# Optimization experiments

Measured on AMD Instinct MI355X. Metric: run time of the kernel, lower is better.

The kernel has to match this reference:

```python
import jax, jax.numpy as jnp
import numpy as np
import math

B, N, D = 8, 4096, 768
H, M, L = 12, 64, 4
HD = D // H  # 64
TEMP = 1.0
EPS = 1e-5


def layer_norm(x, g, b):
    m = jnp.mean(x, axis=-1, keepdims=True)
    v = jnp.mean((x - m) ** 2, axis=-1, keepdims=True)
    return (x - m) * jax.lax.rsqrt(v + EPS) * g + b


def setup_inputs() -> dict:
    key = jax.random.key(0)
    ks = jax.random.split(key, 24)
    s = 0.02
    inp = {
        "latent_tokens": jax.random.normal(ks[0], (B, N, D), jnp.float32),
        "selector": jax.random.normal(ks[1], (M, D), jnp.float32) * s,
        "qc": jax.random.normal(ks[2], (L, M, D), jnp.float32) * s,
        "qw": jax.random.normal(ks[3], (L, H, D, HD), jnp.float32) * s,
        "qb": jnp.zeros((L, H, HD), jnp.float32),
        "kw": jax.random.normal(ks[4], (L, H, D, HD), jnp.float32) * s,
        "kb": jnp.zeros((L, H, HD), jnp.float32),
        "vw": jax.random.normal(ks[5], (L, H, D, HD), jnp.float32) * s,
        "vb": jnp.zeros((L, H, HD), jnp.float32),
        "hw": jax.random.normal(ks[6], (L, H, HD, HD), jnp.float32) * s,
        "hb": jnp.zeros((L, H, HD), jnp.float32),
        "ow": jax.random.normal(ks[7], (L, D, D), jnp.float32) * s,
        "ob": jnp.zeros((L, D), jnp.float32),
        "w1": jax.random.normal(ks[8], (L, D, 4 * D), jnp.float32) * s,
        "b1": jnp.zeros((L, 4 * D), jnp.float32),
        "w2": jax.random.normal(ks[9], (L, 4 * D, D), jnp.float32) * s,
        "b2": jnp.zeros((L, D), jnp.float32),
        "g1": jnp.ones((L, D), jnp.float32),
        "beta1": jnp.zeros((L, D), jnp.float32),
        "g2": jnp.ones((L, D), jnp.float32),
        "beta2": jnp.zeros((L, D), jnp.float32),
    }
    return inp


def reference(latent_tokens, selector, qc, qw, qb, kw, kb, vw, vb, hw, hb,
              ow, ob, w1, b1, w2, b2, g1, beta1, g2, beta2):
    scale = 1.0 / math.sqrt(HD)
    # soft-selection pooling of encoder tokens into M pos queries
    logits = jnp.einsum('bnd,md->bmn', latent_tokens, selector)
    weights = jax.nn.softmax(logits / TEMP, axis=-1)
    x = jnp.einsum('bmn,bnd->bmd', weights, latent_tokens)  # [B,M,D]
    for l in range(L):
        queries = qc[l][None] + x                                    # [B,M,D]
        q = jnp.einsum('bmd,hde->bhme', queries, qw[l]) + qb[l][None, :, None, :]
        k = jnp.einsum('bnd,hde->bhne', latent_tokens, kw[l]) + kb[l][None, :, None, :]
        v = jnp.einsum('bnd,hde->bhne', latent_tokens, vw[l]) + vb[l][None, :, None, :]
        attn = jax.nn.softmax(jnp.einsum('bhme,bhne->bhmn', q, k) * scale, axis=-1)
        o = jnp.einsum('bhmn,bhne->bhme', attn, v)                   # [B,H,M,HD]
        o = jnp.einsum('bhme,hef->bhmf', o, hw[l]) + hb[l][None, :, None, :]
        o = o.transpose(0, 2, 1, 3).reshape(o.shape[0], M, D)        # concat heads
        o = o @ ow[l] + ob[l]
        x1 = layer_norm(o + queries, g1[l], beta1[l])
        mlp = jax.nn.gelu(x1 @ w1[l] + b1[l], approximate=False) @ w2[l] + b2[l]
        x = layer_norm(x1 + mlp, g2[l], beta2[l])
    return x
```

## Files before the change

kernel.cpp:

```cpp
#include <hip/hip_runtime.h>
#include <hip/hip_bf16.h>


using bf16 = __hip_bfloat16;
typedef __attribute__((ext_vector_type(8))) __bf16 bf16x8;
typedef __attribute__((ext_vector_type(4))) float f32x4;
typedef unsigned int u32;
typedef __attribute__((ext_vector_type(4))) u32 u32x4;

#define DEVINL __device__ __forceinline__

DEVINL float bf2f(bf16 v) { return __bfloat162float(v); }
DEVINL bf16 f2bf(float v) { return __float2bfloat16(v); }
DEVINL u32 f2bfu(float f) { bf16 h = __float2bfloat16(f); return *(unsigned short*)&h; }
DEVINL float gelu_f(float x) { return 0.5f * x * (1.0f + erff(x * 0.70710678118654752f)); }

DEVINL void async16(const bf16* g, bf16* l) {
  __builtin_amdgcn_global_load_lds(
      (const __attribute__((address_space(1))) u32*)g,
      (__attribute__((address_space(3))) u32*)l, 16, 0, 0);
}

DEVINL u32 xcd_swizzle(u32 id, u32 nwg) {
  u32 q = nwg >> 3, r = nwg & 7;
  u32 xcd = id & 7, pos = id >> 3;
  return xcd * q + (xcd < r ? xcd : r) + pos;
}

__global__ __launch_bounds__(256) void cvt_f2b(const float* in, bf16* out, long n) {
  const long i = ((long)blockIdx.x * 256 + threadIdx.x) * 8;
  if (i >= n) return;
  float4 a = *(const float4*)(in + i);
  float4 b = *(const float4*)(in + i + 4);
  u32 w[4];
  w[0] = f2bfu(a.x) | (f2bfu(a.y) << 16);
  w[1] = f2bfu(a.z) | (f2bfu(a.w) << 16);
  w[2] = f2bfu(b.x) | (f2bfu(b.y) << 16);
  w[3] = f2bfu(b.z) | (f2bfu(b.w) << 16);
  *(u32x4*)(out + i) = *(u32x4*)w;
}

struct GemmKVP {
  const bf16* A;
  const bf16* Bk;
  const bf16* Bv;
  bf16* Ck;
  bf16* Cv;
  const float* biask;
  const float* biasv;
};

__global__ __launch_bounds__(512, 4) void gemm_kv(GemmKVP p) {
  __shared__ __align__(16) bf16 SH[36864];
  bf16* As = SH;
  bf16* Ks = SH + 12288;
  bf16* Vs = SH + 24576;
  const int tid = threadIdx.x;
  const int wave = tid >> 6, lane = tid & 63;

  u32 id = blockIdx.x + 6u * blockIdx.y;
  id = xcd_swizzle(id, 1536);
  const int bn = id % 6;
  const int bm = id / 6;

  const bf16* Ag = p.A + (long)bm * 128 * 768;
  const bf16* Kg = p.Bk + (long)bn * 128 * 768;
  const bf16* Vg = p.Bv + (long)bn * 128 * 768;

  const int cq = (((tid & 3) ^ ((tid >> 3) & 3))) * 8;
  const long ro = (long)(tid >> 2) * 768 + cq;
  const bf16* ga = Ag + ro;
  const bf16* gk = Kg + ro;
  const bf16* gv = Vg + ro;

  const int m_in = lane & 15, q = lane >> 4;
  const int wstream = wave >> 2;
  const int wq = wave & 3;
  const int wm = (wq & 1) * 64, wn = (wq >> 1) * 64;
  const int sw3 = (q ^ ((m_in >> 1) & 3)) << 3;
  f32x4 acc[4][4] = {};
  const int nk = 24;

  auto stage = [&](int s, int ko) {
    async16(ga + ko, As + s * 4096 + tid * 8);
    async16(gk + ko, Ks + s * 4096 + tid * 8);
    async16(gv + ko, Vs + s * 4096 + tid * 8);
  };
  stage(0, 0);
  stage(1, 32);

  for (int k = 0; k < nk; ++k) {
    if (k + 1 < nk) asm volatile("s_waitcnt vmcnt(3)" ::: "memory");
    else            asm volatile("s_waitcnt vmcnt(0)" ::: "memory");
    __builtin_amdgcn_s_barrier();
    if (k + 2 < nk) stage((k + 2) % 3, (k + 2) * 32);
    const bf16* Ac = As + (k % 3) * 4096;
    const bf16* Bc = (wstream == 0 ? Ks : Vs) + (k % 3) * 4096;
    bf16x8 af[4], bfr[4];
#pragma unroll
    for (int i = 0; i < 4; i++)
      af[i] = *(const bf16x8*)(Ac + (wm + i * 16 + m_in) * 32 + sw3);
#pragma unroll
    for (int j = 0; j < 4; j++)
      bfr[j] = *(const bf16x8*)(Bc + (wn + j * 16 + m_in) * 32 + sw3);
#pragma unroll
    for (int i = 0; i < 4; i++)
#pragma unroll
      for (int j = 0; j < 4; j++)
        acc[i][j] = __builtin_amdgcn_mfma_f32_16x16x32_bf16(af[i], bfr[j], acc[i][j], 0, 0, 0);
  }

  const int bb = (bm * 128) >> 12;
  const int nn0 = (bm * 128) & 4095;
  __syncthreads();
  if (wstream == 0) {
    const long row0 = (long)bm * 128 + wm + q * 4;
    const long col0 = (long)bn * 128 + wn + m_in;
#pragma unroll
    for (int i = 0; i < 4; i++)
#pragma unroll
      for (int j = 0; j < 4; j++) {
        long r = row0 + i * 16;
        long c = col0 + j * 16;
        float bk_ = p.biask[c];
#pragma unroll
        for (int t = 0; t < 4; t++)
          p.Ck[(r + t) * 768 + c] = f2bf(acc[i][j][t] + bk_);
      }
  } else {
    bf16* VT = SH;
#pragma unroll
    for (int i = 0; i < 4; i++) {
      const int nb = wm + q * 4 + i * 16;
      const int sl = nb >> 3;
      const int of = nb & 7;
#pragma unroll
      for (int j = 0; j < 4; j++) {
        const int e = wn + j * 16 + m_in;
        const float bv_ = p.biasv[bn * 128 + e];
        u32 w0 = f2bfu(acc[i][j][0] + bv_) | (f2bfu(acc[i][j][1] + bv_) << 16);
        u32 w1 = f2bfu(acc[i][j][2] + bv_) | (f2bfu(acc[i][j][3] + bv_) << 16);
        uint2 pk; pk.x = w0; pk.y = w1;
        *(uint2*)(VT + e * 128 + ((sl ^ (e & 15)) << 3) + of) = pk;
      }
    }
  }
  __syncthreads();
  bf16* CvB = p.Cv + (long)bb * 3145728;
  const bf16* VT = SH;
#pragma unroll
  for (int k2 = 0; k2 < 4; k2++) {
    int g = tid + k2 * 512;
    int e = g >> 4, sc = g & 15;
    u32x4 vv = *(const u32x4*)(VT + e * 128 + ((sc ^ (e & 15)) << 3));
    *(u32x4*)(CvB + (long)(bn * 128 + e) * 4096 + nn0 + sc * 8) = vv;
  }
}

struct GemmSmP {
  const bf16* A; const bf16* B; void* C; const float* bias; const float* res;
  long sA1, sA2, sB1, sB2, sC1, sC2, sBias2;
  int nb2, lda, ldb, ldc, K;
  int bias_mode;
  int out_mode;
  float scale;
};

__global__ __launch_bounds__(256, 4) void gemm_sm(GemmSmP p) {
  __shared__ __align__(16) bf16 As[3][64 * 32];
  __shared__ __align__(16) bf16 Bs[3][64 * 32];
  const int tid = threadIdx.x;
  const int wave = tid >> 6, lane = tid & 63;

  const u32 gx = gridDim.x, gy = gridDim.y;
  u32 id = blockIdx.x + gx * (blockIdx.y + gy * blockIdx.z);
  id = xcd_swizzle(id, gx * gy * gridDim.z);
  const int bn = id % gx;
  const u32 t2 = id / gx;
  const int bm = t2 % gy;
  const int bz = t2 / gy;

  const int z1 = bz / p.nb2, z2 = bz - z1 * p.nb2;
  const bf16* Ag = p.A + p.sA1 * z1 + p.sA2 * z2 + (long)bm * 64 * p.lda;
  const bf16* Bg = p.B + p.sB1 * z1 + p.sB2 * z2 + (long)bn * 64 * p.ldb;

  const int cq = (((tid & 3) ^ ((tid >> 3) & 3))) * 8;
  const bf16* gpa = Ag + ((long)(tid >> 2) * p.lda + cq);
  const bf16* gpb = Bg + ((long)(tid >> 2) * p.ldb + cq);

  const int m_in = lane & 15, q = lane >> 4;
  const int wm = (wave & 1) * 32, wn = (wave >> 1) * 32;
  const int sw3 = (q ^ ((m_in >> 1) & 3)) << 3;
  f32x4 acc[2][2] = {};
  const int nk = p.K >> 5;

  async16(gpa, &As[0][0] + tid * 8);
  async16(gpb, &Bs[0][0] + tid * 8);
  if (nk > 1) {
    async16(gpa + 32, &As[1][0] + tid * 8);
    async16(gpb + 32, &Bs[1][0] + tid * 8);
  }

  int slot = 0;
  for (int k = 0; k < nk; ++k) {
    if (k + 1 < nk) asm volatile("s_waitcnt vmcnt(2)" ::: "memory");
    else            asm volatile("s_waitcnt vmcnt(0)" ::: "memory");
    __builtin_amdgcn_s_barrier();
    if (k + 2 < nk) {
      int ns = slot + 2; if (ns >= 3) ns -= 3;
      const int ko = (k + 2) * 32;
      async16(gpa + ko, &As[ns][0] + tid * 8);
      async16(gpb + ko, &Bs[ns][0] + tid * 8);
    }
    const bf16* Ac = &As[slot][0];
    const bf16* Bc = &Bs[slot][0];
    bf16x8 a0 = *(const bf16x8*)(Ac + (wm + m_in) * 32 + sw3);
    bf16x8 a1 = *(const bf16x8*)(Ac + (wm + 16 + m_in) * 32 + sw3);
    bf16x8 b0 = *(const bf16x8*)(Bc + (wn + m_in) * 32 + sw3);
    bf16x8 b1 = *(const bf16x8*)(Bc + (wn + 16 + m_in) * 32 + sw3);
    acc[0][0] = __builtin_amdgcn_mfma_f32_16x16x32_bf16(a0, b0, acc[0][0], 0, 0, 0);
    acc[0][1] = __builtin_amdgcn_mfma_f32_16x16x32_bf16(a0, b1, acc[0][1], 0, 0, 0);
    acc[1][0] = __builtin_amdgcn_mfma_f32_16x16x32_bf16(a1, b0, acc[1][0], 0, 0, 0);
    acc[1][1] = __builtin_amdgcn_mfma_f32_16x16x32_bf16(a1, b1, acc[1][1], 0, 0, 0);
    slot = (slot + 1 == 3) ? 0 : slot + 1;
  }

  const long row0 = (long)bm * 64 + wm + q * 4;
  const long col0 = (long)bn * 64 + wn + m_in;
  const float* bias = p.bias + p.sBias2 * z2;
#pragma unroll
  for (int i = 0; i < 2; i++)
#pragma unroll
    for (int j = 0; j < 2; j++) {
      long r = row0 + i * 16;
      long cc = col0 + j * 16;
      float badd = (p.bias_mode == 1) ? bias[cc] : 0.f;
#pragma unroll
      for (int t = 0; t < 4; t++) {
        float v = acc[i][j][t] * p.scale + badd;
        long idx = (r + t) * p.ldc + cc;
        if (p.out_mode == 0) {
          float* Cf = (float*)p.C + p.sC1 * z1 + p.sC2 * z2;
          if (p.res) v += p.res[idx];
          Cf[idx] = v;
        } else {
          bf16* Cb = (bf16*)p.C + p.sC1 * z1 + p.sC2 * z2;
          if (p.out_mode == 2) v = gelu_f(v);
          Cb[idx] = f2bf(v);
        }
      }
    }
}

struct AttnP {
  const bf16* Q;
  const bf16* K;
  const bf16* VT;
  float* Opart;
  float* ML;
};

__global__ __launch_bounds__(256, 3) void attn_part(AttnP p) {
  __shared__ __align__(16) bf16 SH[24576];
  bf16* Qs = SH;
  bf16* Ks = SH + 4096;
  bf16* Vs = SH + 12288;
  bf16* Ps = SH + 20480;
  const int tid = threadIdx.x;
  const int wave = tid >> 6, lane = tid & 63;
  const int z = blockIdx.x, c = blockIdx.y;
  const int b = z / 12, h = z - b * 12;
  const int n0 = c * 512;

  const int sl0 = tid, sl1 = tid + 256;
  const int r0 = sl0 >> 3, r1 = sl1 >> 3;
  const int q0 = (sl0 & 7) ^ (r0 & 7), q1 = (sl1 & 7) ^ (r1 & 7);

  const bf16* Qg = p.Q + ((long)b * 64) * 768 + h * 64;
  const bf16* Kg = p.K + ((long)b * 4096 + n0) * 768 + h * 64;
  const bf16* Vg = p.VT + (long)b * 3145728 + (long)(h * 64) * 4096 + n0;

  async16(Qg + (long)r0 * 768 + q0 * 8, Qs + sl0 * 8);
  async16(Qg + (long)r1 * 768 + q1 * 8, Qs + sl1 * 8);
  auto stageK = [&](int s) {
    bf16* d = Ks + (s & 1) * 4096;
    async16(Kg + (long)(s * 64 + r0) * 768 + q0 * 8, d + sl0 * 8);
    async16(Kg + (long)(s * 64 + r1) * 768 + q1 * 8, d + sl1 * 8);
  };
  auto stageV = [&](int s) {
    bf16* d = Vs + (s & 1) * 4096;
    async16(Vg + (long)r0 * 4096 + s * 64 + q0 * 8, d + sl0 * 8);
    async16(Vg + (long)r1 * 4096 + s * 64 + q1 * 8, d + sl1 * 8);
  };
  stageK(0); stageV(0); stageK(1); stageV(1);

  const int m_in = lane & 15, q = lane >> 4;
  const int wm = wave * 16;

  asm volatile("s_waitcnt vmcnt(8)" ::: "memory");
  __builtin_amdgcn_s_barrier();

  bf16x8 qa[2];
  {
    const int ra = wm + m_in;
#pragma unroll
    for (int kk = 0; kk < 2; kk++)
      qa[kk] = *(const bf16x8*)(Qs + ra * 64 + ((((kk * 4 + q) ^ (ra & 7))) << 3));
  }

  f32x4 accO[4] = {};
  float m_run[4] = {-1e30f, -1e30f, -1e30f, -1e30f};
  float l_run[4] = {0.f, 0.f, 0.f, 0.f};

  for (int s = 0; s < 8; ++s) {
    if (s < 7) asm volatile("s_waitcnt vmcnt(4)" ::: "memory");
    else       asm volatile("s_waitcnt vmcnt(0)" ::: "memory");
    __builtin_amdgcn_s_barrier();
    const bf16* Kc = Ks + (s & 1) * 4096;
    const bf16* Vc = Vs + (s & 1) * 4096;
    f32x4 accS[4] = {};
#pragma unroll
    for (int kk = 0; kk < 2; kk++) {
#pragma unroll
      for (int j = 0; j < 4; j++) {
        const int rj = j * 16 + m_in;
        bf16x8 kb = *(const bf16x8*)(Kc + rj * 64 + ((((kk * 4 + q) ^ (rj & 7))) << 3));
        accS[j] = __builtin_amdgcn_mfma_f32_16x16x32_bf16(qa[kk], kb, accS[j], 0, 0, 0);
      }
    }
    float pe[4][4], osc[4];
#pragma unroll
    for (int t = 0; t < 4; t++) {
      float mx = fmaxf(fmaxf(accS[0][t], accS[1][t]), fmaxf(accS[2][t], accS[3][t])) * 0.125f;
      mx = fmaxf(mx, __shfl_xor(mx, 1));
      mx = fmaxf(mx, __shfl_xor(mx, 2));
      mx = fmaxf(mx, __shfl_xor(mx, 4));
      mx = fmaxf(mx, __shfl_xor(mx, 8));
      const float mnew = fmaxf(m_run[t], mx);
      const float so = __expf(m_run[t] - mnew);
      float rs = 0.f;
#pragma unroll
      for (int j = 0; j < 4; j++) {
        float e = __expf(accS[j][t] * 0.125f - mnew);
        pe[j][t] = e; rs += e;
      }
      rs += __shfl_xor(rs, 1); rs += __shfl_xor(rs, 2);
      rs += __shfl_xor(rs, 4); rs += __shfl_xor(rs, 8);
      l_run[t] = l_run[t] * so + rs;
      m_run[t] = mnew;
      osc[t] = so;
    }
#pragma unroll
    for (int ef = 0; ef < 4; ef++)
#pragma unroll
      for (int t = 0; t < 4; t++) accO[ef][t] *= osc[t];
#pragma unroll
    for (int j = 0; j < 4; j++) {
      const int pc = m_in + 16 * j;
#pragma unroll
      for (int t = 0; t < 4; t++) {
        const int pm = wm + q * 4 + t;
        Ps[pm * 64 + (((pc >> 3) ^ (pm & 7)) << 3) + (pc & 7)] = f2bf(pe[j][t]);
      }
    }
    const int ra = wm + m_in;
#pragma unroll
    for (int kk = 0; kk < 2; kk++) {
      bf16x8 pa = *(const bf16x8*)(Ps + ra * 64 + ((((kk * 4 + q) ^ (ra & 7))) << 3));
#pragma unroll
      for (int ef = 0; ef < 4; ef++) {
        const int rv = ef * 16 + m_in;
        bf16x8 vb = *(const bf16x8*)(Vc + rv * 64 + ((((kk * 4 + q) ^ (rv & 7))) << 3));
        accO[ef] = __builtin_amdgcn_mfma_f32_16x16x32_bf16(pa, vb, accO[ef], 0, 0, 0);
      }
    }
    __builtin_amdgcn_s_barrier();
    if (s < 6) { stageK(s + 2); stageV(s + 2); }
  }

  float* Og = p.Opart + ((long)c * 96 + z) * 4096;
#pragma unroll
  for (int ef = 0; ef < 4; ef++)
#pragma unroll
    for (int t = 0; t < 4; t++)
      Og[(wm + q * 4 + t) * 64 + ef * 16 + m_in] = accO[ef][t];
  if (m_in == 0) {
    float* ml = p.ML + ((long)c * 96 + z) * 128;
#pragma unroll
    for (int t = 0; t < 4; t++) {
      ml[wm + q * 4 + t] = m_run[t];
      ml[64 + wm + q * 4 + t] = l_run[t];
    }
  }
}

struct AttnHMP {
  const float* Opart;
  const float* ML;
  const bf16* HWT;
  const float* hb;
  bf16* O2;
};

__global__ __launch_bounds__(256) void attn_hm(AttnHMP p) {
  __shared__ __align__(16) bf16 Os[4096];
  __shared__ __align__(16) bf16 Hs[4096];
  const int tid = threadIdx.x;
  const int z = blockIdx.x;
  const int b = z / 12, h = z - b * 12;

  const int sl0 = tid, sl1 = tid + 256;
  const int r0 = sl0 >> 3, r1 = sl1 >> 3;
  const int q0 = (sl0 & 7) ^ (r0 & 7), q1 = (sl1 & 7) ^ (r1 & 7);
  const bf16* Hg = p.HWT + h * 4096;
  async16(Hg + r0 * 64 + q0 * 8, Hs + sl0 * 8);
  async16(Hg + r1 * 64 + q1 * 8, Hs + sl1 * 8);

  const int m = tid >> 2, e0 = (tid & 3) * 16;
  float mv[8];
  float mx = -1e30f;
#pragma unroll
  for (int c = 0; c < 8; c++) {
    mv[c] = p.ML[((long)c * 96 + z) * 128 + m];
    mx = fmaxf(mx, mv[c]);
  }
  float l = 0.f;
  float o[16] = {};
#pragma unroll
  for (int c = 0; c < 8; c++) {
    const float w = __expf(mv[c] - mx);
    l += w * p.ML[((long)c * 96 + z) * 128 + 64 + m];
    const float* Og = p.Opart + (((long)c * 96 + z) * 64 + m) * 64 + e0;
#pragma unroll
    for (int e = 0; e < 16; e++) o[e] += w * Og[e];
  }
  const float inv = 1.f / l;
#pragma unroll
  for (int half = 0; half < 2; half++) {
    u32 wbuf[4];
#pragma unroll
    for (int j = 0; j < 4; j++)
      wbuf[j] = f2bfu(o[half * 8 + 2 * j] * inv) | (f2bfu(o[half * 8 + 2 * j + 1] * inv) << 16);
    const int sl = (e0 >> 3) + half;
    *(u32x4*)(Os + m * 64 + ((sl ^ (m & 7)) << 3)) = *(u32x4*)wbuf;
  }
  asm volatile("s_waitcnt vmcnt(0)" ::: "memory");
  __syncthreads();

  const int wave = tid >> 6, lane = tid & 63;
  const int m_in = lane & 15, q = lane >> 4;
  const int wm = wave * 16;
  f32x4 acc[4] = {};
#pragma unroll
  for (int kk = 0; kk < 2; kk++) {
    const int ra = wm + m_in;
    bf16x8 a = *(const bf16x8*)(Os + ra * 64 + ((((kk * 4 + q) ^ (ra & 7))) << 3));
#pragma unroll
    for (int j = 0; j < 4; j++) {
      const int rb = j * 16 + m_in;
      bf16x8 bv = *(const bf16x8*)(Hs + rb * 64 + ((((kk * 4 + q) ^ (rb & 7))) << 3));
      acc[j] = __builtin_amdgcn_mfma_f32_16x16x32_bf16(a, bv, acc[j], 0, 0, 0);
    }
  }
  bf16* O2r = p.O2 + ((long)b * 64) * 768 + h * 64;
#pragma unroll
  for (int j = 0; j < 4; j++) {
    const int e2 = j * 16 + m_in;
    const float badd = p.hb[h * 64 + e2];
#pragma unroll
    for (int t = 0; t < 4; t++)
      O2r[(wm + q * 4 + t) * 768 + e2] = f2bf(acc[j][t] + badd);
  }
}

struct TrP { const float* in; bf16* out; bf16* outR; int R, C; long sIn, sOut, sOutR; };

__global__ __launch_bounds__(256) void transpose_f2b(TrP p) {
  __shared__ __align__(16) bf16 tile[64][80];
  const int tid = threadIdx.x;
  const int ct = blockIdx.x, rt = blockIdx.y, z = blockIdx.z;
  const float* in = p.in + p.sIn * z + ((long)rt * 64) * p.C + (long)ct * 64;
  bf16* out = p.out + p.sOut * z + ((long)ct * 64) * p.R + (long)rt * 64;
  bf16* outR = p.outR ? p.outR + p.sOutR * z + ((long)rt * 64) * p.C + (long)ct * 64 : nullptr;
  const int r = tid >> 3, c8 = (tid & 7) * 8;
#pragma unroll
  for (int h = 0; h < 2; h++) {
    int rr = r + h * 32;
    float4 a = *(const float4*)(in + (long)rr * p.C + c8);
    float4 b = *(const float4*)(in + (long)rr * p.C + c8 + 4);
    u32 w[4];
    w[0] = f2bfu(a.x) | (f2bfu(a.y) << 16);
    w[1] = f2bfu(a.z) | (f2bfu(a.w) << 16);
    w[2] = f2bfu(b.x) | (f2bfu(b.y) << 16);
    w[3] = f2bfu(b.z) | (f2bfu(b.w) << 16);
    *(u32x4*)&tile[rr][c8] = *(u32x4*)w;
    if (outR) *(u32x4*)(outR + (long)rr * p.C + c8) = *(u32x4*)w;
  }
  __syncthreads();
  const int co = tid >> 3, r8 = (tid & 7) * 8;
#pragma unroll
  for (int h = 0; h < 2; h++) {
    int cc = co + h * 32;
    __align__(16) bf16 tmp[8];
#pragma unroll
    for (int j = 0; j < 8; j++) tmp[j] = tile[r8 + j][cc];
    *(u32x4*)(out + (long)cc * p.R + r8) = *(const u32x4*)tmp;
  }
}

__global__ __launch_bounds__(256) void softmax_rows(bf16* X) {
  const long row = blockIdx.x;
  u32* x = (u32*)(X + row * 4096);
  const int tid = threadIdx.x;
  const int lane = tid & 63, wave = tid >> 6;
  u32 d[8];
  *(u32x4*)&d[0] = ((const u32x4*)x)[tid * 2];
  *(u32x4*)&d[4] = ((const u32x4*)x)[tid * 2 + 1];
  float v[16];
#pragma unroll
  for (int j = 0; j < 8; j++) {
    v[2 * j] = __uint_as_float(d[j] << 16);
    v[2 * j + 1] = __uint_as_float(d[j] & 0xffff0000u);
  }
  float m = v[0];
#pragma unroll
  for (int i = 1; i < 16; i++) m = fmaxf(m, v[i]);
  for (int off = 32; off; off >>= 1) m = fmaxf(m, __shfl_xor(m, off));
  __shared__ float sm1[4], sm2[4];
  if (lane == 0) sm1[wave] = m;
  __syncthreads();
  m = fmaxf(fmaxf(sm1[0], sm1[1]), fmaxf(sm1[2], sm1[3]));
  float s = 0.f;
#pragma unroll
  for (int i = 0; i < 16; i++) { v[i] = __expf(v[i] - m); s += v[i]; }
  for (int off = 32; off; off >>= 1) s += __shfl_xor(s, off);
  if (lane == 0) sm2[wave] = s;
  __syncthreads();
  s = sm2[0] + sm2[1] + sm2[2] + sm2[3];
  const float inv = 1.f / s;
#pragma unroll
  for (int j = 0; j < 8; j++) {
    u32 lo = f2bfu(v[2 * j] * inv);
    u32 hi = f2bfu(v[2 * j + 1] * inv);
    d[j] = lo | (hi << 16);
  }
  ((u32x4*)x)[tid * 2] = *(u32x4*)&d[0];
  ((u32x4*)x)[tid * 2 + 1] = *(u32x4*)&d[4];
}

struct CombLnP {
  const float* in; int nch; const float* bias; const float* res;
  const float* g; const float* b;
  float* outf; bf16* outb;
  const float* qc; float* qf; bf16* qb16;
};

__global__ __launch_bounds__(256) void comb_ln(CombLnP p) {
  const long row = blockIdx.x;
  const long base = row * 768;
  const int tid = threadIdx.x;
  const int lane = tid & 63, wave = tid >> 6;
  float v0 = 0.f, v1 = 0.f, v2 = 0.f;
  for (int c = 0; c < p.nch; c++) {
    const float* x = p.in + (long)c * 393216 + base;
    v0 += x[tid]; v1 += x[tid + 256]; v2 += x[tid + 512];
  }
  v0 += p.bias[tid]; v1 += p.bias[tid + 256]; v2 += p.bias[tid + 512];
  if (p.res) {
    const float* r = p.res + base;
    v0 += r[tid]; v1 += r[tid + 256]; v2 += r[tid + 512];
  }
  float s = v0 + v1 + v2;
  float s2 = v0 * v0 + v1 * v1 + v2 * v2;
  for (int off = 32; off; off >>= 1) { s += __shfl_xor(s, off); s2 += __shfl_xor(s2, off); }
  __shared__ float sa[4], sb[4];
  if (lane == 0) { sa[wave] = s; sb[wave] = s2; }
  __syncthreads();
  s = sa[0] + sa[1] + sa[2] + sa[3];
  s2 = sb[0] + sb[1] + sb[2] + sb[3];
  const float mean = s * (1.f / 768.f);
  const float var = s2 * (1.f / 768.f) - mean * mean;
  const float rs = rsqrtf(var + 1e-5f);
  float o0 = (v0 - mean) * rs * p.g[tid] + p.b[tid];
  float o1 = (v1 - mean) * rs * p.g[tid + 256] + p.b[tid + 256];
  float o2 = (v2 - mean) * rs * p.g[tid + 512] + p.b[tid + 512];
  if (p.outf) { float* of = p.outf + base; of[tid] = o0; of[tid + 256] = o1; of[tid + 512] = o2; }
  if (p.outb) { bf16* ob = p.outb + base; ob[tid] = f2bf(o0); ob[tid + 256] = f2bf(o1); ob[tid + 512] = f2bf(o2); }
  if (p.qc) {
    const float* qr = p.qc + (row & 63) * 768;
    float u0 = o0 + qr[tid], u1 = o1 + qr[tid + 256], u2 = o2 + qr[tid + 512];
    float* pf = p.qf + base;
    pf[tid] = u0; pf[tid + 256] = u1; pf[tid + 512] = u2;
    bf16* pb = p.qb16 + base;
    pb[tid] = f2bf(u0); pb[tid + 256] = f2bf(u1); pb[tid + 512] = f2bf(u2);
  }
}

struct CombP { const float* in; int nch; const float* bias; const float* res;
               float* outf; bf16* outb; const float* qc; float* qf; bf16* qb16; };

__global__ __launch_bounds__(256) void combine(CombP p) {
  const long i = (long)blockIdx.x * 256 + threadIdx.x;
  float s = 0.f;
  for (int c = 0; c < p.nch; c++) s += p.in[(long)c * 393216 + i];
  if (p.bias) s += p.bias[i % 768];
  if (p.res) s += p.res[i];
  if (p.outf) p.outf[i] = s;
  if (p.outb) p.outb[i] = f2bf(s);
  if (p.qc) {
    float v = s + p.qc[i % 49152];
    p.qf[i] = v;
    p.qb16[i] = f2bf(v);
  }
}

extern "C" void kernel_launch(void* const* d_in, const int* in_sizes, int n_in,
                              void* d_out, int out_size, void* d_ws, size_t ws_size,
                              hipStream_t stream) {
  (void)in_sizes; (void)n_in; (void)out_size; (void)ws_size;
  const float* tokens   = (const float*)d_in[0];
  const float* selector = (const float*)d_in[1];
  const float* qc  = (const float*)d_in[2];
  const float* qw  = (const float*)d_in[3];
  const float* qb  = (const float*)d_in[4];
  const float* kw  = (const float*)d_in[5];
  const float* kb  = (const float*)d_in[6];
  const float* vw  = (const float*)d_in[7];
  const float* vb  = (const float*)d_in[8];
  const float* hw  = (const float*)d_in[9];
  const float* hb  = (const float*)d_in[10];
  const float* ow  = (const float*)d_in[11];
  const float* ob  = (const float*)d_in[12];
  const float* w1  = (const float*)d_in[13];
  const float* b1  = (const float*)d_in[14];
  const float* w2  = (const float*)d_in[15];
  const float* b2  = (const float*)d_in[16];
  const float* g1  = (const float*)d_in[17];
  const float* be1 = (const float*)d_in[18];
  const float* g2  = (const float*)d_in[19];
  const float* be2 = (const float*)d_in[20];
  float* out = (float*)d_out;

  char* ws = (char*)d_ws;
  size_t off = 0;
  auto alloc = [&](size_t bytes) { char* pp = ws + off; off += (bytes + 255) & ~(size_t)255; return pp; };
  bf16* TOKT  = (bf16*)alloc(50331648);
  bf16* TOKB  = (bf16*)alloc(50331648);
  bf16* KBUF  = (bf16*)alloc(50331648);
  bf16* VTB   = (bf16*)alloc(50331648);
  bf16* PLOG  = (bf16*)alloc(4194304);
  bf16* SELB  = (bf16*)alloc(98304);
  bf16* QWT   = (bf16*)alloc(4718592);
  bf16* KWT   = (bf16*)alloc(4718592);
  bf16* VWT   = (bf16*)alloc(4718592);
  bf16* HWT   = (bf16*)alloc(393216);
  bf16* OWT   = (bf16*)alloc(4718592);
  bf16* W1T   = (bf16*)alloc(18874368);
  bf16* W2T   = (bf16*)alloc(18874368);
  bf16* QBUF  = (bf16*)alloc(786432);
  bf16* O2BUF = (bf16*)alloc(786432);
  float* QF   = (float*)alloc(1572864);
  bf16* QB16  = (bf16*)alloc(786432);
  float* X1F  = (float*)alloc(1572864);
  bf16* X1B   = (bf16*)alloc(786432);
  bf16* H1    = (bf16*)alloc(3145728);
  float* OPART = (float*)alloc(12582912);
  float* MLB  = (float*)alloc(393216);

  auto tr = [&](const float* in, bf16* o, bf16* oR, int R, int C, long s, long sR, int slabs) {
    TrP t{in, o, oR, R, C, s, s, sR};
    transpose_f2b<<<dim3(C / 64, R / 64, slabs), 256, 0, stream>>>(t);
  };
  tr(tokens, TOKT, TOKB, 4096, 768, 3145728, 3145728, 8);
  cvt_f2b<<<24, 256, 0, stream>>>(selector, SELB, 49152);
  tr(qw, QWT, nullptr, 768, 64, 49152, 0, 48);
  tr(kw, KWT, nullptr, 768, 64, 49152, 0, 48);
  tr(vw, VWT, nullptr, 768, 64, 49152, 0, 48);
  tr(hw, HWT, nullptr, 64, 64, 4096, 0, 48);
  tr(ow, OWT, nullptr, 768, 768, 589824, 0, 4);
  tr(w1, W1T, nullptr, 768, 3072, 2359296, 0, 4);
  tr(w2, W2T, nullptr, 3072, 768, 2359296, 0, 4);

  {
    GemmSmP p{}; p.A = SELB; p.B = TOKB; p.C = PLOG;
    p.sB1 = 3145728; p.sC1 = 262144; p.nb2 = 1;
    p.lda = 768; p.ldb = 768; p.ldc = 4096; p.K = 768;
    p.bias_mode = 0; p.out_mode = 1; p.scale = 1.0f;
    gemm_sm<<<dim3(64, 1, 8), 256, 0, stream>>>(p);
  }
  softmax_rows<<<512, 256, 0, stream>>>(PLOG);
  {
    GemmSmP p{}; p.A = PLOG; p.B = TOKT; p.C = OPART;
    p.sA1 = 512; p.sA2 = 262144; p.sB1 = 512; p.sB2 = 3145728;
    p.sC1 = 393216; p.sC2 = 49152; p.nb2 = 8;
    p.lda = 4096; p.ldb = 4096; p.ldc = 768; p.K = 512;
    p.bias_mode = 0; p.out_mode = 0; p.scale = 1.0f;
    gemm_sm<<<dim3(12, 1, 64), 256, 0, stream>>>(p);
  }
  {
    CombP c{}; c.in = OPART; c.nch = 8; c.qc = qc; c.qf = QF; c.qb16 = QB16;
    combine<<<1536, 256, 0, stream>>>(c);
  }

  for (int l = 0; l < 4; l++) {
    {
      GemmSmP p{}; p.A = QB16; p.B = QWT + l * 589824; p.C = QBUF; p.bias = qb + l * 768;
      p.nb2 = 1; p.lda = 768; p.ldb = 768; p.ldc = 768; p.K = 768;
      p.bias_mode = 1; p.out_mode = 1; p.scale = 1.0f;
      gemm_sm<<<dim3(12, 8, 1), 256, 0, stream>>>(p);
    }
    {
      GemmKVP p{TOKB, KWT + l * 589824, VWT + l * 589824, KBUF, VTB,
                kb + l * 768, vb + l * 768};
      gemm_kv<<<dim3(6, 256, 1), 512, 0, stream>>>(p);
    }
    {
      AttnP p{QBUF, KBUF, VTB, OPART, MLB};
      attn_part<<<dim3(96, 8, 1), 256, 0, stream>>>(p);
    }
    {
      AttnHMP p{OPART, MLB, HWT + l * 49152, hb + l * 768, O2BUF};
      attn_hm<<<96, 256, 0, stream>>>(p);
    }
    {
      GemmSmP p{}; p.A = O2BUF; p.B = OWT + l * 589824; p.C = OPART;
      p.sA1 = 192; p.sB1 = 192; p.sC1 = 393216; p.nb2 = 1;
      p.lda = 768; p.ldb = 768; p.ldc = 768; p.K = 192;
      p.bias_mode = 0; p.out_mode = 0; p.scale = 1.0f;
      gemm_sm<<<dim3(12, 8, 4), 256, 0, stream>>>(p);
    }
    {
      CombLnP c{}; c.in = OPART; c.nch = 4; c.bias = ob + l * 768; c.res = QF;
      c.g = g1 + l * 768; c.b = be1 + l * 768; c.outf = X1F; c.outb = X1B;
      comb_ln<<<512, 256, 0, stream>>>(c);
    }
    {
      GemmSmP p{}; p.A = X1B; p.B = W1T + l * 2359296; p.C = H1; p.bias = b1 + l * 3072;
      p.nb2 = 1; p.lda = 768; p.ldb = 768; p.ldc = 3072; p.K = 768;
      p.bias_mode = 1; p.out_mode = 2; p.scale = 1.0f;
      gemm_sm<<<dim3(48, 8, 1), 256, 0, stream>>>(p);
    }
    {
      GemmSmP p{}; p.A = H1; p.B = W2T + l * 2359296; p.C = OPART;
      p.sA1 = 384; p.sB1 = 384; p.sC1 = 393216; p.nb2 = 1;
      p.lda = 3072; p.ldb = 3072; p.ldc = 768; p.K = 384;
      p.bias_mode = 0; p.out_mode = 0; p.scale = 1.0f;
      gemm_sm<<<dim3(12, 8, 8), 256, 0, stream>>>(p);
    }
    {
      CombLnP c{}; c.in = OPART; c.nch = 8; c.bias = b2 + l * 768; c.res = X1F;
      c.g = g2 + l * 768; c.b = be2 + l * 768;
      c.outf = (l == 3) ? out : nullptr;
      c.qc = (l < 3) ? (qc + (l + 1) * 49152) : nullptr;
      c.qf = QF; c.qb16 = QB16;
      comb_ln<<<512, 256, 0, stream>>>(c);
    }
  }
}
```

Baseline: 1.057 ms.

## Fold Q projection into KV GEMM launch and batch weight transposes

The per-layer Q projection GEMM now runs as 24 extra blocks appended to the gemm_kv grid, which removes one launch per layer and lets the small Q GEMM overlap with the large KV GEMM. Those Q blocks compute a redundant second stream whose result is discarded. The three Q/K/V weight transposes are merged into a single launch that relies on QWT, KWT and VWT sitting contiguously in memory. s_setprio is also raised around the MFMA sections in the attention kernel to help wave scheduling.

```diff
diff --git a/kernel.cpp b/kernel.cpp
--- a/kernel.cpp
+++ b/kernel.cpp
@@ -48,6 +48,10 @@
   bf16* Cv;
   const float* biask;
   const float* biasv;
+  const bf16* Aq;
+  const bf16* Bq;
+  bf16* Cq;
+  const float* biasq;
 };
 
 __global__ __launch_bounds__(512, 4) void gemm_kv(GemmKVP p) {
@@ -58,14 +62,16 @@
   const int tid = threadIdx.x;
   const int wave = tid >> 6, lane = tid & 63;
 
-  u32 id = blockIdx.x + 6u * blockIdx.y;
-  id = xcd_swizzle(id, 1536);
-  const int bn = id % 6;
-  const int bm = id / 6;
-
-  const bf16* Ag = p.A + (long)bm * 128 * 768;
-  const bf16* Kg = p.Bk + (long)bn * 128 * 768;
-  const bf16* Vg = p.Bv + (long)bn * 128 * 768;
+  u32 id = blockIdx.x;
+  id = xcd_swizzle(id, 1560);
+  const bool qblk = id >= 1536;
+  const u32 rid = qblk ? id - 1536 : id;
+  const int bn = rid % 6;
+  const int bm = rid / 6;
+
+  const bf16* Ag = (qblk ? p.Aq : p.A) + (long)bm * 128 * 768;
+  const bf16* Kg = (qblk ? p.Bq : p.Bk) + (long)bn * 128 * 768;
+  const bf16* Vg = (qblk ? p.Bq : p.Bv) + (long)bn * 128 * 768;
 
   const int cq = (((tid & 3) ^ ((tid >> 3) & 3))) * 8;
   const long ro = (long)(tid >> 2) * 768 + cq;
@@ -108,6 +114,25 @@
 #pragma unroll
       for (int j = 0; j < 4; j++)
         acc[i][j] = __builtin_amdgcn_mfma_f32_16x16x32_bf16(af[i], bfr[j], acc[i][j], 0, 0, 0);
+  }
+
+  if (qblk) {
+    if (wstream == 0) {
+      const long row0 = (long)bm * 128 + wm + q * 4;
+      const long col0 = (long)bn * 128 + wn + m_in;
+#pragma unroll
+      for (int i = 0; i < 4; i++)
+#pragma unroll
+        for (int j = 0; j < 4; j++) {
+          long r = row0 + i * 16;
+          long c = col0 + j * 16;
+          float bq_ = p.biasq[c];
+#pragma unroll
+          for (int t = 0; t < 4; t++)
+            p.Cq[(r + t) * 768 + c] = f2bf(acc[i][j][t] + bq_);
+        }
+    }
+    return;
   }
 
   const int bb = (bm * 128) >> 12;
@@ -319,6 +344,7 @@
     const bf16* Kc = Ks + (s & 1) * 4096;
     const bf16* Vc = Vs + (s & 1) * 4096;
     f32x4 accS[4] = {};
+    __builtin_amdgcn_s_setprio(1);
 #pragma unroll
     for (int kk = 0; kk < 2; kk++) {
 #pragma unroll
@@ -328,6 +354,7 @@
         accS[j] = __builtin_amdgcn_mfma_f32_16x16x32_bf16(qa[kk], kb, accS[j], 0, 0, 0);
       }
     }
+    __builtin_amdgcn_s_setprio(0);
     float pe[4][4], osc[4];
 #pragma unroll
     for (int t = 0; t < 4; t++) {
@@ -364,6 +391,7 @@
       }
     }
     const int ra = wm + m_in;
+    __builtin_amdgcn_s_setprio(1);
 #pragma unroll
     for (int kk = 0; kk < 2; kk++) {
       bf16x8 pa = *(const bf16x8*)(Ps + ra * 64 + ((((kk * 4 + q) ^ (ra & 7))) << 3));
@@ -374,6 +402,7 @@
         accO[ef] = __builtin_amdgcn_mfma_f32_16x16x32_bf16(pa, vb, accO[ef], 0, 0, 0);
       }
     }
+    __builtin_amdgcn_s_setprio(0);
     __builtin_amdgcn_s_barrier();
     if (s < 6) { stageK(s + 2); stageV(s + 2); }
   }
@@ -473,13 +502,22 @@
   }
 }
 
-struct TrP { const float* in; bf16* out; bf16* outR; int R, C; long sIn, sOut, sOutR; };
+struct TrP { const float* in; bf16* out; bf16* outR; int R, C; long sIn, sOut, sOutR;
+             const float* in2; const float* in3; };
 
 __global__ __launch_bounds__(256) void transpose_f2b(TrP p) {
   __shared__ __align__(16) bf16 tile[64][80];
   const int tid = threadIdx.x;
   const int ct = blockIdx.x, rt = blockIdx.y, z = blockIdx.z;
-  const float* in = p.in + p.sIn * z + ((long)rt * 64) * p.C + (long)ct * 64;
+  const float* src = p.in;
+  int zz = z;
+  if (p.in2) {
+    const int g = z / 48;
+    zz = z - g * 48;
+    if (g == 1) src = p.in2;
+    else if (g == 2) src = p.in3;
+  }
+  const float* in = src + p.sIn * zz + ((long)rt * 64) * p.C + (long)ct * 64;
   bf16* out = p.out + p.sOut * z + ((long)ct * 64) * p.R + (long)rt * 64;
   bf16* outR = p.outR ? p.outR + p.sOutR * z + ((long)rt * 64) * p.C + (long)ct * 64 : nullptr;
   const int r = tid >> 3, c8 = (tid & 7) * 8;
@@ -666,16 +704,18 @@
   bf16* H1    = (bf16*)alloc(3145728);
   float* OPART = (float*)alloc(12582912);
   float* MLB  = (float*)alloc(393216);
+  (void)KWT; (void)VWT;
 
   auto tr = [&](const float* in, bf16* o, bf16* oR, int R, int C, long s, long sR, int slabs) {
-    TrP t{in, o, oR, R, C, s, s, sR};
+    TrP t{in, o, oR, R, C, s, s, sR, nullptr, nullptr};
     transpose_f2b<<<dim3(C / 64, R / 64, slabs), 256, 0, stream>>>(t);
   };
   tr(tokens, TOKT, TOKB, 4096, 768, 3145728, 3145728, 8);
   cvt_f2b<<<24, 256, 0, stream>>>(selector, SELB, 49152);
-  tr(qw, QWT, nullptr, 768, 64, 49152, 0, 48);
-  tr(kw, KWT, nullptr, 768, 64, 49152, 0, 48);
-  tr(vw, VWT, nullptr, 768, 64, 49152, 0, 48);
+  {
+    TrP t{qw, QWT, nullptr, 768, 64, 49152, 49152, 0, kw, vw};
+    transpose_f2b<<<dim3(1, 12, 144), 256, 0, stream>>>(t);
+  }
   tr(hw, HWT, nullptr, 64, 64, 4096, 0, 48);
   tr(ow, OWT, nullptr, 768, 768, 589824, 0, 4);
   tr(w1, W1T, nullptr, 768, 3072, 2359296, 0, 4);
@@ -704,15 +744,10 @@
 
   for (int l = 0; l < 4; l++) {
     {
-      GemmSmP p{}; p.A = QB16; p.B = QWT + l * 589824; p.C = QBUF; p.bias = qb + l * 768;
-      p.nb2 = 1; p.lda = 768; p.ldb = 768; p.ldc = 768; p.K = 768;
-      p.bias_mode = 1; p.out_mode = 1; p.scale = 1.0f;
-      gemm_sm<<<dim3(12, 8, 1), 256, 0, stream>>>(p);
-    }
-    {
-      GemmKVP p{TOKB, KWT + l * 589824, VWT + l * 589824, KBUF, VTB,
-                kb + l * 768, vb + l * 768};
-      gemm_kv<<<dim3(6, 256, 1), 512, 0, stream>>>(p);
+      GemmKVP p{TOKB, QWT + 2359296 + l * 589824, QWT + 2 * 2359296 + l * 589824,
+                KBUF, VTB, kb + l * 768, vb + l * 768,
+                QB16, QWT + l * 589824, QBUF, qb + l * 768};
+      gemm_kv<<<1560, 512, 0, stream>>>(p);
     }
     {
       AttnP p{QBUF, KBUF, VTB, OPART, MLB};
```

Measured after the change: 1.034 ms. 2.2% less time.
